# Kernel optimization log

Hardware: AMD Instinct MI355X
Metric: run time of the kernel (lower is better)

The kernel has to match this reference:

```python
import jax, jax.numpy as jnp
import numpy as np

EMBED_DIM = 1024
NUM_HEADS = 16
HEAD_DIM = EMBED_DIM // NUM_HEADS
FF_DIM = 4 * EMBED_DIM
LN_EPS = 1e-5


def setup_inputs() -> dict:
    key = jax.random.key(0)
    ks = jax.random.split(key, 17)
    s = 0.02
    d = EMBED_DIM
    return {
        "x": jax.random.normal(ks[0], (2, 2048, d), dtype=jnp.float32),
        "Wq": jax.random.normal(ks[1], (d, d), dtype=jnp.float32) * s,
        "bq": jnp.zeros((d,), dtype=jnp.float32),
        "Wk": jax.random.normal(ks[2], (d, d), dtype=jnp.float32) * s,
        "bk": jnp.zeros((d,), dtype=jnp.float32),
        "Wv": jax.random.normal(ks[3], (d, d), dtype=jnp.float32) * s,
        "bv": jnp.zeros((d,), dtype=jnp.float32),
        "Wo": jax.random.normal(ks[4], (d, d), dtype=jnp.float32) * s,
        "bo": jnp.zeros((d,), dtype=jnp.float32),
        "W1": jax.random.normal(ks[5], (d, FF_DIM), dtype=jnp.float32) * s,
        "b1": jnp.zeros((FF_DIM,), dtype=jnp.float32),
        "W2": jax.random.normal(ks[6], (FF_DIM, d), dtype=jnp.float32) * s,
        "b2": jnp.zeros((d,), dtype=jnp.float32),
        "g1": jnp.ones((d,), dtype=jnp.float32),
        "beta1": jnp.zeros((d,), dtype=jnp.float32),
        "g2": jnp.ones((d,), dtype=jnp.float32),
        "beta2": jnp.zeros((d,), dtype=jnp.float32),
    }


def _layer_norm(x, g, b):
    mu = jnp.mean(x, axis=-1, keepdims=True)
    var = jnp.var(x, axis=-1, keepdims=True)
    return (x - mu) * jax.lax.rsqrt(var + LN_EPS) * g + b


def _mhsa(x, Wq, bq, Wk, bk, Wv, bv, Wo, bo):
    B, S, D = x.shape
    q = (x @ Wq + bq).reshape(B, S, NUM_HEADS, HEAD_DIM)
    k = (x @ Wk + bk).reshape(B, S, NUM_HEADS, HEAD_DIM)
    v = (x @ Wv + bv).reshape(B, S, NUM_HEADS, HEAD_DIM)
    # NOTE: original module applies NO 1/sqrt(head_dim) scaling
    scores = jnp.einsum("bqhd,bkhd->bhqk", q, k)  # [B,H,S,S]
    attn = jax.nn.softmax(scores, axis=-1)
    out = jnp.einsum("bhqk,bkhd->bqhd", attn, v).reshape(B, S, D)
    return out @ Wo + bo


def reference(x, Wq, bq, Wk, bk, Wv, bv, Wo, bo, W1, b1, W2, b2, g1, beta1, g2, beta2):
    x = x + _mhsa(x, Wq, bq, Wk, bk, Wv, bv, Wo, bo)
    x = _layer_norm(x, g1, beta1)
    h = jax.nn.gelu(x @ W1 + b1, approximate=False)
    x = x + (h @ W2 + b2)
    x = _layer_norm(x, g2, beta2)
    return x
```

## Files before the change

kernel.cpp:

```cpp
#include <hip/hip_runtime.h>
#include <math.h>

#define SEQ 2048
#define NBATCH 2
#define NHEAD 16
#define HDIM 64
#define DMODEL 1024
#define DFF 4096

typedef __attribute__((ext_vector_type(8))) __bf16 bf16x8;
typedef __attribute__((ext_vector_type(4))) float f32x4;

__device__ __forceinline__ unsigned short f2bf(float f) {
    union { __bf16 b; unsigned short u; } c;
    c.b = (__bf16)f;
    return c.u;
}

__device__ __forceinline__ void async16(const unsigned short* g, unsigned short* l) {
    __builtin_amdgcn_global_load_lds(
        (const __attribute__((address_space(1))) unsigned int*)(g),
        (__attribute__((address_space(3))) unsigned int*)(l),
        16, 0, 0);
}

__device__ __forceinline__ void transpose_tile(
    const float* __restrict__ in, unsigned short* __restrict__ out,
    int K, int N, int k0, int n0, int t, unsigned short* sT)
{
    {
        const int r = t >> 4, c4 = t & 15;
#pragma unroll
        for (int i = 0; i < 4; i++) {
            const int k = r + (i << 4);
            const float4 v = *(const float4*)(in + (size_t)(k0 + k) * N + n0 + (c4 << 2));
            sT[((c4 << 2) + 0) * 72 + k] = f2bf(v.x);
            sT[((c4 << 2) + 1) * 72 + k] = f2bf(v.y);
            sT[((c4 << 2) + 2) * 72 + k] = f2bf(v.z);
            sT[((c4 << 2) + 3) * 72 + k] = f2bf(v.w);
        }
    }
    __syncthreads();
    {
        const int n = t >> 2, cc = t & 3;
#pragma unroll
        for (int i = 0; i < 2; i++) {
            const int c = cc + (i << 2);
            *(uint4*)(out + (size_t)(n0 + n) * K + k0 + (c << 3)) =
                *(const uint4*)(&sT[n * 72 + (c << 3)]);
        }
    }
}

__global__ __launch_bounds__(256) void prep_kernel(
    const float* __restrict__ x,
    const float* __restrict__ Wq, const float* __restrict__ Wk,
    const float* __restrict__ Wv, const float* __restrict__ Wo,
    const float* __restrict__ W1, const float* __restrict__ W2,
    const float* __restrict__ bq, const float* __restrict__ bk,
    const float* __restrict__ bv,
    unsigned short* __restrict__ xb, unsigned short* __restrict__ WqkvT,
    unsigned short* __restrict__ WoT, unsigned short* __restrict__ W1T,
    unsigned short* __restrict__ W2T, float* __restrict__ bqkv)
{
    __shared__ unsigned short sT[64 * 72];
    const int bid = blockIdx.x, t = threadIdx.x;
    if (bid < 1024) {
        const int wsel = bid >> 8, tt = bid & 255;
        const float* in = (wsel == 0) ? Wq : (wsel == 1) ? Wk : (wsel == 2) ? Wv : Wo;
        unsigned short* outp = (wsel == 3) ? WoT : WqkvT + (size_t)wsel * 1024 * 1024;
        transpose_tile(in, outp, 1024, 1024, (tt >> 4) << 6, (tt & 15) << 6, t, sT);
    } else if (bid < 2048) {
        const int tt = bid - 1024;
        transpose_tile(W1, W1T, 1024, 4096, (tt >> 6) << 6, (tt & 63) << 6, t, sT);
    } else if (bid < 3072) {
        const int tt = bid - 2048;
        transpose_tile(W2, W2T, 4096, 1024, (tt >> 4) << 6, (tt & 15) << 6, t, sT);
    } else if (bid < 7168) {
        const size_t i = ((size_t)(bid - 3072) * 256 + t) << 2;
        const float4 v = *(const float4*)(x + i);
        ushort4 b;
        b.x = f2bf(v.x); b.y = f2bf(v.y); b.z = f2bf(v.z); b.w = f2bf(v.w);
        *(ushort4*)(xb + i) = b;
    } else {
        const int i = (bid - 7168) * 256 + t;
        float v;
        if (i < 1024)       v = bq[i];
        else if (i < 2048)  v = bk[i - 1024];
        else                v = bv[i - 2048];
        bqkv[i] = v;
    }
}

template<int EPI>
__global__ __launch_bounds__(256) void gemm_bf16_kernel(
    const unsigned short* __restrict__ A, const unsigned short* __restrict__ Bt,
    const float* __restrict__ bias, float* __restrict__ outF,
    unsigned short* __restrict__ outB, unsigned short* __restrict__ outQ,
    unsigned short* __restrict__ outK, unsigned short* __restrict__ outV,
    int N, int K, size_t pstride)
{
    __shared__ unsigned short sA[128 * 64];
    __shared__ unsigned short sB[128 * 64];
    const int gx = gridDim.x, gy = gridDim.y;
    const int flat = blockIdx.y * gx + blockIdx.x;
    const int xcd = flat & 7, slot = flat >> 3;
    const int rx = gx >> 1, ry = gy >> 2;
    const int bx = (xcd & 1) * rx + (slot % rx);
    const int by = (xcd >> 1) * ry + (slot / rx);
    const int m0 = by << 7;
    const int n0 = bx << 7;
    const int kspan = K / gridDim.z;
    const int kbeg = blockIdx.z * kspan;

    const int t = threadIdx.x;
    const int w = t >> 6, l = t & 63, li = l & 15, quad = l >> 4;
    const int wm = (w >> 1) << 6, wn = (w & 1) << 6;
    const int srow = l >> 3;
    const int scol = ((l & 7) ^ srow) << 3;

    f32x4 acc[4][4];
#pragma unroll
    for (int mi = 0; mi < 4; mi++)
#pragma unroll
        for (int ni = 0; ni < 4; ni++)
            acc[mi][ni] = (f32x4){0.f, 0.f, 0.f, 0.f};

    for (int k0 = kbeg; k0 < kbeg + kspan; k0 += 64) {
#pragma unroll
        for (int i = 0; i < 4; i++) {
            const int c = (w << 2) + i;
            async16(A  + (size_t)(m0 + (c << 3) + srow) * K + k0 + scol, &sA[c << 9]);
            async16(Bt + (size_t)(n0 + (c << 3) + srow) * K + k0 + scol, &sB[c << 9]);
        }
        __syncthreads();
#pragma unroll
        for (int ks = 0; ks < 2; ks++) {
            bf16x8 af[4], bfr[4];
#pragma unroll
            for (int mi = 0; mi < 4; mi++)
                af[mi] = *(const bf16x8*)(&sA[((wm + (mi << 4) + li) << 6) +
                                             ((((ks << 2) + quad) ^ (li & 7)) << 3)]);
#pragma unroll
            for (int ni = 0; ni < 4; ni++)
                bfr[ni] = *(const bf16x8*)(&sB[((wn + (ni << 4) + li) << 6) +
                                              ((((ks << 2) + quad) ^ (li & 7)) << 3)]);
#pragma unroll
            for (int mi = 0; mi < 4; mi++)
#pragma unroll
                for (int ni = 0; ni < 4; ni++)
                    acc[mi][ni] = __builtin_amdgcn_mfma_f32_16x16x32_bf16(
                        af[mi], bfr[ni], acc[mi][ni], 0, 0, 0);
        }
        __syncthreads();
    }

    if (EPI == 0) {
        const int region = n0 >> 10;
        const int bq_ = m0 >> 11;
        const int sloc = (m0 & 2047) + wm + (quad << 2);
        const float qscale = (region == 0) ? 1.4426950408889634f : 1.0f;
#pragma unroll
        for (int ni = 0; ni < 4; ni++) {
            const int col = n0 + wn + (ni << 4) + li;
            const int c = col & 1023;
            const int h = c >> 6, d = c & 63;
            const float bcol = bias[col];
            if (region < 2) {
                unsigned short* base = ((region == 0) ? outQ : outK) +
                    (((size_t)(bq_ * NHEAD + h)) << 17) + d;
#pragma unroll
                for (int mi = 0; mi < 4; mi++)
#pragma unroll
                    for (int r = 0; r < 4; r++)
                        base[(size_t)(sloc + (mi << 4) + r) << 6] =
                            f2bf((acc[mi][ni][r] + bcol) * qscale);
            } else {
                unsigned short* base = outV + (((size_t)(bq_ * NHEAD + h)) << 17) +
                    ((size_t)d << 11) + sloc;
#pragma unroll
                for (int mi = 0; mi < 4; mi++) {
                    ushort4 pk;
                    pk.x = f2bf(acc[mi][ni][0] + bcol);
                    pk.y = f2bf(acc[mi][ni][1] + bcol);
                    pk.z = f2bf(acc[mi][ni][2] + bcol);
                    pk.w = f2bf(acc[mi][ni][3] + bcol);
                    *(ushort4*)(base + (mi << 4)) = pk;
                }
            }
        }
    } else {
        float* outFz = outF + (size_t)blockIdx.z * pstride;
#pragma unroll
        for (int mi = 0; mi < 4; mi++) {
#pragma unroll
            for (int ni = 0; ni < 4; ni++) {
#pragma unroll
                for (int r = 0; r < 4; r++) {
                    const int row = m0 + wm + (mi << 4) + (quad << 2) + r;
                    const int col = n0 + wn + (ni << 4) + li;
                    float v = acc[mi][ni][r];
                    if (EPI == 2) {
                        v += bias[col];
                        const float u = v * v;
                        const float wq = fmaf(-0.1029432f, u, -2.30220786f);
                        const float e = __builtin_amdgcn_exp2f(v * wq);
                        const float ge = v * __builtin_amdgcn_rcpf(1.0f + e);
                        outB[(size_t)row * N + col] = f2bf(ge);
                    } else {
                        outFz[(size_t)row * N + col] = v;
                    }
                }
            }
        }
    }
}

__global__ __launch_bounds__(256) void attn_kernel(
    const unsigned short* __restrict__ Qb, const unsigned short* __restrict__ Kb,
    const unsigned short* __restrict__ Vt, unsigned short* __restrict__ AOb)
{
    __shared__ unsigned short sK[2][64 * 64];
    __shared__ unsigned short sV[2][64 * 64];
    __shared__ unsigned short sP[4][16 * 64];
    const int t = threadIdx.x, w = t >> 6, l = t & 63;
    const int li = l & 15, quad = l >> 4;
    const int p = blockIdx.x;
    const int xcd = p & 7, slot = p >> 3;
    const int bh = (xcd << 2) + (slot >> 5);
    const int q0 = (slot & 31) << 6;
    const unsigned short* Qh = Qb + ((size_t)bh << 17);
    const unsigned short* Kh = Kb + ((size_t)bh << 17);
    const unsigned short* Vh = Vt + ((size_t)bh << 17);
    const int qw = q0 + (w << 4);
    const int ssw = ((l & 7) ^ (l >> 3)) << 3;
    const int lq7 = li & 7;

    bf16x8 bq[2];
#pragma unroll
    for (int h = 0; h < 2; h++)
        bq[h] = *(const bf16x8*)(Qh + ((size_t)(qw + li) << 6) + (h << 5) + (quad << 3));

    bf16x8 bone;
#pragma unroll
    for (int j = 0; j < 8; j++) bone[j] = (__bf16)1.0f;

    f32x4 o[4];
    f32x4 accl = (f32x4){0.f, 0.f, 0.f, 0.f};
#pragma unroll
    for (int d = 0; d < 4; d++) o[d] = (f32x4){0.f, 0.f, 0.f, 0.f};
    const f32x4 z = (f32x4){0.f, 0.f, 0.f, 0.f};
    unsigned short* myP = &sP[w][0];

    unsigned short* wp[4];
#pragma unroll
    for (int nt = 0; nt < 4; nt++)
        wp[nt] = myP + (li << 6) +
                 ((((nt << 1) + (quad >> 1)) ^ lq7) << 3) + ((quad & 1) << 2);

#define STAGE(buf, kc)                                                              \
    {                                                                               \
        _Pragma("unroll")                                                           \
        for (int i = 0; i < 4; i++) {                                               \
            const int cc = (w << 2) + i;                                            \
            if (cc < 8)                                                             \
                async16(Kh + ((size_t)((kc) + (cc << 3) + (l >> 3)) << 6) + ssw,    \
                        &sK[buf][cc << 9]);                                         \
            else                                                                    \
                async16(Vh + ((size_t)(((cc - 8) << 3) + (l >> 3)) << 11) + (kc) + ssw, \
                        &sV[buf][(cc - 8) << 9]);                                   \
        }                                                                           \
    }

    STAGE(0, 0);
    __syncthreads();

    for (int kc = 0, it = 0; kc < SEQ; kc += 64, it++) {
        const int cur = it & 1;
        if (kc + 64 < SEQ) STAGE(cur ^ 1, kc + 64);

#pragma unroll
        for (int nt = 0; nt < 4; nt++) {
            const bf16x8 ak0 = *(const bf16x8*)(&sK[cur][(((nt << 4) + li) << 6) +
                                                         ((quad ^ lq7) << 3)]);
            const bf16x8 ak1 = *(const bf16x8*)(&sK[cur][(((nt << 4) + li) << 6) +
                                                         (((4 + quad) ^ lq7) << 3)]);
            f32x4 sc = __builtin_amdgcn_mfma_f32_16x16x32_bf16(ak0, bq[0], z, 0, 0, 0);
            sc = __builtin_amdgcn_mfma_f32_16x16x32_bf16(ak1, bq[1], sc, 0, 0, 0);
            ushort4 pk;
            pk.x = f2bf(__builtin_amdgcn_exp2f(sc[0]));
            pk.y = f2bf(__builtin_amdgcn_exp2f(sc[1]));
            pk.z = f2bf(__builtin_amdgcn_exp2f(sc[2]));
            pk.w = f2bf(__builtin_amdgcn_exp2f(sc[3]));
            *(ushort4*)wp[nt] = pk;
        }

        bf16x8 ap[2];
#pragma unroll
        for (int h = 0; h < 2; h++)
            ap[h] = *(const bf16x8*)(myP + (li << 6) + ((((h << 2) + quad) ^ lq7) << 3));

        accl = __builtin_amdgcn_mfma_f32_16x16x32_bf16(ap[0], bone, accl, 0, 0, 0);
        accl = __builtin_amdgcn_mfma_f32_16x16x32_bf16(ap[1], bone, accl, 0, 0, 0);
#pragma unroll
        for (int dt = 0; dt < 4; dt++) {
#pragma unroll
            for (int h = 0; h < 2; h++) {
                const bf16x8 bv = *(const bf16x8*)(&sV[cur][(((dt << 4) + li) << 6) +
                                                            ((((h << 2) + quad) ^ lq7) << 3)]);
                o[dt] = __builtin_amdgcn_mfma_f32_16x16x32_bf16(ap[h], bv, o[dt], 0, 0, 0);
            }
        }
        __syncthreads();
    }

    const int b = bh >> 4, h = bh & 15;
    float inv[4];
#pragma unroll
    for (int r = 0; r < 4; r++) inv[r] = __builtin_amdgcn_rcpf(accl[r]);
#pragma unroll
    for (int dt = 0; dt < 4; dt++)
#pragma unroll
        for (int r = 0; r < 4; r++) {
            const int row = qw + (quad << 2) + r;
            const int col = (h << 6) + (dt << 4) + li;
            AOb[((size_t)b * SEQ + row) * DMODEL + col] = f2bf(o[dt][r] * inv[r]);
        }
}

__global__ __launch_bounds__(256) void ln_fuse_kernel(
    const float* __restrict__ P0, const float* __restrict__ P1,
    const float* __restrict__ resid, const float* __restrict__ bias,
    const float* __restrict__ g, const float* __restrict__ be,
    float* __restrict__ outF, unsigned short* __restrict__ outB)
{
    __shared__ float red[8];
    const int row = blockIdx.x, t = threadIdx.x;
    const size_t base = (size_t)row * DMODEL + (t << 2);
    const float4 a = *(const float4*)(P0 + base);
    const float4 b = *(const float4*)(P1 + base);
    const float4 c = *(const float4*)(resid + base);
    const float4 bi = *(const float4*)(bias + (t << 2));
    float4 v;
    v.x = a.x + b.x + c.x + bi.x;
    v.y = a.y + b.y + c.y + bi.y;
    v.z = a.z + b.z + c.z + bi.z;
    v.w = a.w + b.w + c.w + bi.w;
    float s = v.x + v.y + v.z + v.w;
    float s2 = v.x * v.x + v.y * v.y + v.z * v.z + v.w * v.w;
#pragma unroll
    for (int m = 1; m < 64; m <<= 1) {
        s += __shfl_xor(s, m, 64);
        s2 += __shfl_xor(s2, m, 64);
    }
    if ((t & 63) == 0) { red[t >> 6] = s; red[4 + (t >> 6)] = s2; }
    __syncthreads();
    s = red[0] + red[1] + red[2] + red[3];
    s2 = red[4] + red[5] + red[6] + red[7];
    const float mu = s * (1.0f / 1024.0f);
    const float var = s2 * (1.0f / 1024.0f) - mu * mu;
    const float rs = rsqrtf(var + 1e-5f);
    const float4 gg = *(const float4*)(g + (t << 2));
    const float4 bb = *(const float4*)(be + (t << 2));
    float4 ov;
    ov.x = (v.x - mu) * rs * gg.x + bb.x;
    ov.y = (v.y - mu) * rs * gg.y + bb.y;
    ov.z = (v.z - mu) * rs * gg.z + bb.z;
    ov.w = (v.w - mu) * rs * gg.w + bb.w;
    *(float4*)(outF + base) = ov;
    if (outB) {
        ushort4 ob;
        ob.x = f2bf(ov.x); ob.y = f2bf(ov.y); ob.z = f2bf(ov.z); ob.w = f2bf(ov.w);
        *(ushort4*)(outB + base) = ob;
    }
}

extern "C" void kernel_launch(void* const* d_in, const int* in_sizes, int n_in,
                              void* d_out, int out_size, void* d_ws, size_t ws_size,
                              hipStream_t stream)
{
    (void)in_sizes; (void)n_in; (void)out_size; (void)ws_size;
    const float* x   = (const float*)d_in[0];
    const float* Wq  = (const float*)d_in[1];
    const float* bq  = (const float*)d_in[2];
    const float* Wk  = (const float*)d_in[3];
    const float* bk  = (const float*)d_in[4];
    const float* Wv  = (const float*)d_in[5];
    const float* bv  = (const float*)d_in[6];
    const float* Wo  = (const float*)d_in[7];
    const float* bo  = (const float*)d_in[8];
    const float* W1  = (const float*)d_in[9];
    const float* b1  = (const float*)d_in[10];
    const float* W2  = (const float*)d_in[11];
    const float* b2  = (const float*)d_in[12];
    const float* g1  = (const float*)d_in[13];
    const float* be1 = (const float*)d_in[14];
    const float* g2  = (const float*)d_in[15];
    const float* be2 = (const float*)d_in[16];
    float* out = (float*)d_out;

    char* ws = (char*)d_ws;
    unsigned short* WqkvT = (unsigned short*)(ws + 0);
    unsigned short* WoT   = (unsigned short*)(ws + 6291456);
    unsigned short* W1T   = (unsigned short*)(ws + 8388608);
    unsigned short* W2T   = (unsigned short*)(ws + 16777216);
    float* bqkv           = (float*)(ws + 25165824);
    unsigned short* xb    = (unsigned short*)(ws + 25178112);
    unsigned short* Qb    = (unsigned short*)(ws + 33566720);
    unsigned short* Kb    = (unsigned short*)(ws + 41955328);
    unsigned short* Vt    = (unsigned short*)(ws + 50343936);
    unsigned short* AOb   = (unsigned short*)(ws + 58732544);
    float* x1             = (float*)(ws + 67121152);
    unsigned short* x1b   = (unsigned short*)(ws + 83898368);
    unsigned short* hb    = (unsigned short*)(ws + 92286976);
    float* Po0 = (float*)(ws + 92286976);
    float* Po1 = (float*)(ws + 92286976 + 16777216);
    float* Pf0 = (float*)(ws + 33566720);
    float* Pf1 = (float*)(ws + 50343936);

    prep_kernel<<<7180, 256, 0, stream>>>(
        x, Wq, Wk, Wv, Wo, W1, W2, bq, bk, bv,
        xb, WqkvT, WoT, W1T, W2T, bqkv);

    gemm_bf16_kernel<0><<<dim3(24, 32), 256, 0, stream>>>(
        xb, WqkvT, bqkv, nullptr, nullptr, Qb, Kb, Vt, 3072, 1024, 0);

    attn_kernel<<<1024, 256, 0, stream>>>(Qb, Kb, Vt, AOb);

    gemm_bf16_kernel<3><<<dim3(8, 32, 2), 256, 0, stream>>>(
        AOb, WoT, nullptr, Po0, nullptr, nullptr, nullptr, nullptr, 1024, 1024,
        (size_t)4096 * 1024);

    ln_fuse_kernel<<<4096, 256, 0, stream>>>(Po0, Po1, x, bo, g1, be1, x1, x1b);

    gemm_bf16_kernel<2><<<dim3(32, 32), 256, 0, stream>>>(
        x1b, W1T, b1, nullptr, hb, nullptr, nullptr, nullptr, 4096, 1024, 0);

    gemm_bf16_kernel<3><<<dim3(8, 32, 2), 256, 0, stream>>>(
        hb, W2T, nullptr, Pf0, nullptr, nullptr, nullptr, nullptr, 1024, 4096,
        (size_t)4096 * 1024);

    ln_fuse_kernel<<<4096, 256, 0, stream>>>(Pf0, Pf1, x1, b2, g2, be2, out, nullptr);
}
```

Before: 353.5 us.

## Double query rows per attention wave and drop fp32 LN1 output

Each attention wave now processes 32 query rows instead of 16, so every K/V tile staged in shared memory is reused across twice as many queries and the grid is halved to 512 blocks. Separately, the first layernorm no longer writes an fp32 copy, and the second layernorm reads the residual from the bf16 copy instead. Together these are meant to cut K/V staging traffic per query and about 16 MB of fp32 write and read. In exchange, register pressure and occupancy in attention change, fewer blocks may underfill the GPU, and the residual now carries bf16 rounding error.

```diff
diff --git a/kernel.cpp b/kernel.cpp
--- a/kernel.cpp
+++ b/kernel.cpp
@@ -15,6 +15,11 @@
     union { __bf16 b; unsigned short u; } c;
     c.b = (__bf16)f;
     return c.u;
+}
+__device__ __forceinline__ float bf2f(unsigned short u) {
+    union { unsigned int u; float f; } c;
+    c.u = ((unsigned int)u) << 16;
+    return c.f;
 }
 
 __device__ __forceinline__ void async16(const unsigned short* g, unsigned short* l) {
@@ -222,41 +227,50 @@
 {
     __shared__ unsigned short sK[2][64 * 64];
     __shared__ unsigned short sV[2][64 * 64];
-    __shared__ unsigned short sP[4][16 * 64];
+    __shared__ unsigned short sP[4][32 * 64];
     const int t = threadIdx.x, w = t >> 6, l = t & 63;
     const int li = l & 15, quad = l >> 4;
     const int p = blockIdx.x;
     const int xcd = p & 7, slot = p >> 3;
-    const int bh = (xcd << 2) + (slot >> 5);
-    const int q0 = (slot & 31) << 6;
+    const int bh = (xcd << 2) + (slot >> 4);
+    const int q0 = (slot & 15) << 7;
     const unsigned short* Qh = Qb + ((size_t)bh << 17);
     const unsigned short* Kh = Kb + ((size_t)bh << 17);
     const unsigned short* Vh = Vt + ((size_t)bh << 17);
-    const int qw = q0 + (w << 4);
+    const int qw = q0 + (w << 5);
     const int ssw = ((l & 7) ^ (l >> 3)) << 3;
     const int lq7 = li & 7;
 
-    bf16x8 bq[2];
-#pragma unroll
-    for (int h = 0; h < 2; h++)
-        bq[h] = *(const bf16x8*)(Qh + ((size_t)(qw + li) << 6) + (h << 5) + (quad << 3));
+    bf16x8 bq[2][2];
+#pragma unroll
+    for (int m = 0; m < 2; m++)
+#pragma unroll
+        for (int h = 0; h < 2; h++)
+            bq[m][h] = *(const bf16x8*)(Qh + ((size_t)(qw + (m << 4) + li) << 6) +
+                                        (h << 5) + (quad << 3));
 
     bf16x8 bone;
 #pragma unroll
     for (int j = 0; j < 8; j++) bone[j] = (__bf16)1.0f;
 
-    f32x4 o[4];
-    f32x4 accl = (f32x4){0.f, 0.f, 0.f, 0.f};
-#pragma unroll
-    for (int d = 0; d < 4; d++) o[d] = (f32x4){0.f, 0.f, 0.f, 0.f};
+    f32x4 o[2][4];
+    f32x4 accl[2];
+#pragma unroll
+    for (int m = 0; m < 2; m++) {
+        accl[m] = (f32x4){0.f, 0.f, 0.f, 0.f};
+#pragma unroll
+        for (int d = 0; d < 4; d++) o[m][d] = (f32x4){0.f, 0.f, 0.f, 0.f};
+    }
     const f32x4 z = (f32x4){0.f, 0.f, 0.f, 0.f};
     unsigned short* myP = &sP[w][0];
 
-    unsigned short* wp[4];
-#pragma unroll
-    for (int nt = 0; nt < 4; nt++)
-        wp[nt] = myP + (li << 6) +
-                 ((((nt << 1) + (quad >> 1)) ^ lq7) << 3) + ((quad & 1) << 2);
+    unsigned short* wp[2][4];
+#pragma unroll
+    for (int m = 0; m < 2; m++)
+#pragma unroll
+        for (int nt = 0; nt < 4; nt++)
+            wp[m][nt] = myP + (((m << 4) + li) << 6) +
+                        ((((nt << 1) + (quad >> 1)) ^ lq7) << 3) + ((quad & 1) << 2);
 
 #define STAGE(buf, kc)                                                              \
     {                                                                               \
@@ -285,52 +299,68 @@
                                                          ((quad ^ lq7) << 3)]);
             const bf16x8 ak1 = *(const bf16x8*)(&sK[cur][(((nt << 4) + li) << 6) +
                                                          (((4 + quad) ^ lq7) << 3)]);
-            f32x4 sc = __builtin_amdgcn_mfma_f32_16x16x32_bf16(ak0, bq[0], z, 0, 0, 0);
-            sc = __builtin_amdgcn_mfma_f32_16x16x32_bf16(ak1, bq[1], sc, 0, 0, 0);
-            ushort4 pk;
-            pk.x = f2bf(__builtin_amdgcn_exp2f(sc[0]));
-            pk.y = f2bf(__builtin_amdgcn_exp2f(sc[1]));
-            pk.z = f2bf(__builtin_amdgcn_exp2f(sc[2]));
-            pk.w = f2bf(__builtin_amdgcn_exp2f(sc[3]));
-            *(ushort4*)wp[nt] = pk;
-        }
-
-        bf16x8 ap[2];
-#pragma unroll
-        for (int h = 0; h < 2; h++)
-            ap[h] = *(const bf16x8*)(myP + (li << 6) + ((((h << 2) + quad) ^ lq7) << 3));
-
-        accl = __builtin_amdgcn_mfma_f32_16x16x32_bf16(ap[0], bone, accl, 0, 0, 0);
-        accl = __builtin_amdgcn_mfma_f32_16x16x32_bf16(ap[1], bone, accl, 0, 0, 0);
+#pragma unroll
+            for (int m = 0; m < 2; m++) {
+                f32x4 sc = __builtin_amdgcn_mfma_f32_16x16x32_bf16(ak0, bq[m][0], z, 0, 0, 0);
+                sc = __builtin_amdgcn_mfma_f32_16x16x32_bf16(ak1, bq[m][1], sc, 0, 0, 0);
+                ushort4 pk;
+                pk.x = f2bf(__builtin_amdgcn_exp2f(sc[0]));
+                pk.y = f2bf(__builtin_amdgcn_exp2f(sc[1]));
+                pk.z = f2bf(__builtin_amdgcn_exp2f(sc[2]));
+                pk.w = f2bf(__builtin_amdgcn_exp2f(sc[3]));
+                *(ushort4*)wp[m][nt] = pk;
+            }
+        }
+
+        bf16x8 ap[2][2];
+#pragma unroll
+        for (int m = 0; m < 2; m++)
+#pragma unroll
+            for (int h = 0; h < 2; h++)
+                ap[m][h] = *(const bf16x8*)(myP + (((m << 4) + li) << 6) +
+                                            ((((h << 2) + quad) ^ lq7) << 3));
+
+#pragma unroll
+        for (int m = 0; m < 2; m++) {
+            accl[m] = __builtin_amdgcn_mfma_f32_16x16x32_bf16(ap[m][0], bone, accl[m], 0, 0, 0);
+            accl[m] = __builtin_amdgcn_mfma_f32_16x16x32_bf16(ap[m][1], bone, accl[m], 0, 0, 0);
+        }
 #pragma unroll
         for (int dt = 0; dt < 4; dt++) {
 #pragma unroll
             for (int h = 0; h < 2; h++) {
                 const bf16x8 bv = *(const bf16x8*)(&sV[cur][(((dt << 4) + li) << 6) +
                                                             ((((h << 2) + quad) ^ lq7) << 3)]);
-                o[dt] = __builtin_amdgcn_mfma_f32_16x16x32_bf16(ap[h], bv, o[dt], 0, 0, 0);
+#pragma unroll
+                for (int m = 0; m < 2; m++)
+                    o[m][dt] = __builtin_amdgcn_mfma_f32_16x16x32_bf16(ap[m][h], bv, o[m][dt], 0, 0, 0);
             }
         }
         __syncthreads();
     }
 
     const int b = bh >> 4, h = bh & 15;
-    float inv[4];
-#pragma unroll
-    for (int r = 0; r < 4; r++) inv[r] = __builtin_amdgcn_rcpf(accl[r]);
-#pragma unroll
-    for (int dt = 0; dt < 4; dt++)
-#pragma unroll
-        for (int r = 0; r < 4; r++) {
-            const int row = qw + (quad << 2) + r;
-            const int col = (h << 6) + (dt << 4) + li;
-            AOb[((size_t)b * SEQ + row) * DMODEL + col] = f2bf(o[dt][r] * inv[r]);
-        }
-}
-
+#pragma unroll
+    for (int m = 0; m < 2; m++) {
+        float inv[4];
+#pragma unroll
+        for (int r = 0; r < 4; r++) inv[r] = __builtin_amdgcn_rcpf(accl[m][r]);
+#pragma unroll
+        for (int dt = 0; dt < 4; dt++)
+#pragma unroll
+            for (int r = 0; r < 4; r++) {
+                const int row = qw + (m << 4) + (quad << 2) + r;
+                const int col = (h << 6) + (dt << 4) + li;
+                AOb[((size_t)b * SEQ + row) * DMODEL + col] = f2bf(o[m][dt][r] * inv[r]);
+            }
+    }
+}
+
+template<int RESB>
 __global__ __launch_bounds__(256) void ln_fuse_kernel(
     const float* __restrict__ P0, const float* __restrict__ P1,
-    const float* __restrict__ resid, const float* __restrict__ bias,
+    const float* __restrict__ residF, const unsigned short* __restrict__ residB,
+    const float* __restrict__ bias,
     const float* __restrict__ g, const float* __restrict__ be,
     float* __restrict__ outF, unsigned short* __restrict__ outB)
 {
@@ -339,7 +369,13 @@
     const size_t base = (size_t)row * DMODEL + (t << 2);
     const float4 a = *(const float4*)(P0 + base);
     const float4 b = *(const float4*)(P1 + base);
-    const float4 c = *(const float4*)(resid + base);
+    float4 c;
+    if (RESB) {
+        const ushort4 cb = *(const ushort4*)(residB + base);
+        c.x = bf2f(cb.x); c.y = bf2f(cb.y); c.z = bf2f(cb.z); c.w = bf2f(cb.w);
+    } else {
+        c = *(const float4*)(residF + base);
+    }
     const float4 bi = *(const float4*)(bias + (t << 2));
     float4 v;
     v.x = a.x + b.x + c.x + bi.x;
@@ -367,7 +403,7 @@
     ov.y = (v.y - mu) * rs * gg.y + bb.y;
     ov.z = (v.z - mu) * rs * gg.z + bb.z;
     ov.w = (v.w - mu) * rs * gg.w + bb.w;
-    *(float4*)(outF + base) = ov;
+    if (outF) *(float4*)(outF + base) = ov;
     if (outB) {
         ushort4 ob;
         ob.x = f2bf(ov.x); ob.y = f2bf(ov.y); ob.z = f2bf(ov.z); ob.w = f2bf(ov.w);
@@ -410,7 +446,6 @@
     unsigned short* Kb    = (unsigned short*)(ws + 41955328);
     unsigned short* Vt    = (unsigned short*)(ws + 50343936);
     unsigned short* AOb   = (unsigned short*)(ws + 58732544);
-    float* x1             = (float*)(ws + 67121152);
     unsigned short* x1b   = (unsigned short*)(ws + 83898368);
     unsigned short* hb    = (unsigned short*)(ws + 92286976);
     float* Po0 = (float*)(ws + 92286976);
@@ -425,13 +460,14 @@
     gemm_bf16_kernel<0><<<dim3(24, 32), 256, 0, stream>>>(
         xb, WqkvT, bqkv, nullptr, nullptr, Qb, Kb, Vt, 3072, 1024, 0);
 
-    attn_kernel<<<1024, 256, 0, stream>>>(Qb, Kb, Vt, AOb);
+    attn_kernel<<<512, 256, 0, stream>>>(Qb, Kb, Vt, AOb);
 
     gemm_bf16_kernel<3><<<dim3(8, 32, 2), 256, 0, stream>>>(
         AOb, WoT, nullptr, Po0, nullptr, nullptr, nullptr, nullptr, 1024, 1024,
         (size_t)4096 * 1024);
 
-    ln_fuse_kernel<<<4096, 256, 0, stream>>>(Po0, Po1, x, bo, g1, be1, x1, x1b);
+    ln_fuse_kernel<0><<<4096, 256, 0, stream>>>(
+        Po0, Po1, x, nullptr, bo, g1, be1, nullptr, x1b);
 
     gemm_bf16_kernel<2><<<dim3(32, 32), 256, 0, stream>>>(
         x1b, W1T, b1, nullptr, hb, nullptr, nullptr, nullptr, 4096, 1024, 0);
@@ -440,5 +476,6 @@
         hb, W2T, nullptr, Pf0, nullptr, nullptr, nullptr, nullptr, 1024, 4096,
         (size_t)4096 * 1024);
 
-    ln_fuse_kernel<<<4096, 256, 0, stream>>>(Pf0, Pf1, x1, b2, g2, be2, out, nullptr);
-}
+    ln_fuse_kernel<1><<<4096, 256, 0, stream>>>(
+        Pf0, Pf1, nullptr, x1b, b2, g2, be2, out, nullptr);
+}
```

New measurement: 335.7 us. 5.0% less time.
